# Kernel tuning notes

Hardware: AMD Instinct MI355X
Metric: run time of the kernel (lower is better)

Reference implementation:

```python
import jax, jax.numpy as jnp
import numpy as np

B, C, D_IN, T = 8, 4, 256, 1024
D_MODEL = 256


def setup_inputs() -> dict:
    key = jax.random.key(0)
    k_x, k_m, k_wq, k_bq, k_wo, k_bo = jax.random.split(key, 6)
    x = jax.random.normal(k_x, (B, C, D_IN, T), dtype=jnp.float32)
    mask = jax.random.randint(k_m, (B, C, T, T), 0, 2) == 1  # bool, True = masked
    s_in = 1.0 / np.sqrt(D_IN)
    s_md = 1.0 / np.sqrt(D_MODEL)
    w_qkv = jax.random.uniform(k_wq, (3 * D_MODEL, D_IN), jnp.float32, -s_in, s_in)
    b_qkv = jax.random.uniform(k_bq, (3 * D_MODEL,), jnp.float32, -s_in, s_in)
    w_out = jax.random.uniform(k_wo, (D_MODEL, D_MODEL), jnp.float32, -s_md, s_md)
    b_out = jax.random.uniform(k_bo, (D_MODEL,), jnp.float32, -s_md, s_md)
    return {"x": x, "mask": mask, "w_qkv": w_qkv, "b_qkv": b_qkv,
            "w_out": w_out, "b_out": b_out}


def reference(x, mask, w_qkv, b_qkv, w_out, b_out):
    # x: (B, C, d_in, t) -> (B, C, t, d_in)
    xt = jnp.swapaxes(x, -1, -2)
    qkv = jnp.einsum('bctd,ed->bcte', xt, w_qkv) + b_qkv  # (B,C,t,3*d_model)
    q, k, v = jnp.split(qkv, 3, axis=-1)
    scale = 1.0 / jnp.sqrt(jnp.asarray(q.shape[-1], dtype=q.dtype))
    scores = jnp.einsum('bcqd,bckd->bcqk', q, k) * scale  # (B,C,t,t)
    scores = jnp.where(mask, -jnp.inf, scores)
    attn = jax.nn.softmax(scores, axis=-1)
    out = jnp.einsum('bcqk,bckd->bcqd', attn, v)          # (B,C,t,d_model)
    return jnp.einsum('bcqd,ed->bcqe', out, w_out) + b_out
```

## Files before the change

### kernel.cpp

```cpp
#include <hip/hip_runtime.h>
#include <hip/hip_bf16.h>

#define TT 1024
#define DM 256
#define BCN 32

typedef __attribute__((ext_vector_type(8))) short short8;
typedef __attribute__((ext_vector_type(4))) short short4v;
typedef __attribute__((ext_vector_type(4))) float f32x4;

__device__ __forceinline__ void wg_barrier_lds() {
  asm volatile("s_waitcnt lgkmcnt(0)\n\ts_barrier" ::: "memory");
}

__device__ __forceinline__ short bf16b(float f) {
  __hip_bfloat16 h = __float2bfloat16(f);
  return *(short*)&h;
}

__device__ __forceinline__ void dma16(void* l, const void* g) {
  __builtin_amdgcn_global_load_lds(
      (const __attribute__((address_space(1))) void*)g,
      (__attribute__((address_space(3))) void*)l, 16, 0, 0);
}
__device__ __forceinline__ void dma4(void* l, const void* g) {
  __builtin_amdgcn_global_load_lds(
      (const __attribute__((address_space(1))) void*)g,
      (__attribute__((address_space(3))) void*)l, 4, 0, 0);
}

__global__ __launch_bounds__(256, 2) void qkv_kernel(
    const float* __restrict__ x, const float* __restrict__ w_qkv,
    const float* __restrict__ b_qkv, const int* __restrict__ mask,
    __hip_bfloat16* __restrict__ Qb, __hip_bfloat16* __restrict__ Kb,
    __hip_bfloat16* __restrict__ Vtb, unsigned* __restrict__ mbits)
{
  const int tid = threadIdx.x;

  if (blockIdx.x >= 512) {
    const int g = (blockIdx.x - 512) * 256 + tid;
#pragma unroll
    for (int k = 0; k < 8; ++k) {
      const int word = g + k * 131072;
      const int bc = word >> 15, j = (word >> 10) & 31, q = word & 1023;
      const int4* mp =
          (const int4*)(mask + ((size_t)(bc * 1024 + q) * 1024 + j * 32));
      unsigned w = 0;
#pragma unroll
      for (int i = 0; i < 8; ++i) {
        const int4 v = mp[i];
        w |= ((unsigned)(v.x != 0) << (4 * i)) |
             ((unsigned)(v.y != 0) << (4 * i + 1)) |
             ((unsigned)(v.z != 0) << (4 * i + 2)) |
             ((unsigned)(v.w != 0) << (4 * i + 3));
      }
      mbits[word] = w;
    }
    return;
  }

  const int tt = blockIdx.x & 15, bc = blockIdx.x >> 4;
  const int t0 = tt * 64;

  __shared__ __attribute__((aligned(16))) __hip_bfloat16 Xs[64][264];
  __shared__ __attribute__((aligned(16))) __hip_bfloat16 Ws[64][264];

  const int w = tid >> 6, l = tid & 63, quad = l >> 4, lm = l & 15;
  const float* xbc = x + (size_t)bc * DM * TT;

  {
    const int t4 = (tid & 15) * 4;
    for (int s = 0; s < 4; ++s) {
      const int d4 = (tid >> 4) * 4 + s * 64;
      f32x4 f[4];
#pragma unroll
      for (int r = 0; r < 4; ++r)
        f[r] = *(const f32x4*)(xbc + (size_t)(d4 + r) * TT + t0 + t4);
#pragma unroll
      for (int r = 0; r < 4; ++r) {
        short4v pk;
#pragma unroll
        for (int c = 0; c < 4; ++c) pk[c] = bf16b(f[c][r]);
        *(short4v*)&Xs[t4 + r][d4] = pk;
      }
    }
  }

  const float4* wv4 = (const float4*)w_qkv;

  for (int et = 0; et < 12; ++et) {
    const int e0 = et * 64;
    const bool vmode = (et >= 8);
    wg_barrier_lds();
#pragma unroll
    for (int i = 0; i < 16; ++i) {
      const int idx = tid + i * 256, row = idx >> 6, c4 = idx & 63;
      const float4 f = wv4[(size_t)et * 4096 + idx];
      short4v pk;
      pk[0] = bf16b(f.x); pk[1] = bf16b(f.y);
      pk[2] = bf16b(f.z); pk[3] = bf16b(f.w);
      *(short4v*)&Ws[row][c4 * 4] = pk;
    }
    wg_barrier_lds();

    f32x4 acc[4] = {};
#pragma unroll
    for (int ks = 0; ks < 8; ++ks) {
      const int k = ks * 32 + quad * 8;
      const short8 xa = *(const short8*)&Xs[w * 16 + lm][k];
#pragma unroll
      for (int nt = 0; nt < 4; ++nt) {
        const short8 wb = *(const short8*)&Ws[nt * 16 + lm][k];
        acc[nt] = vmode
            ? __builtin_amdgcn_mfma_f32_16x16x32_bf16(xa, wb, acc[nt], 0, 0, 0)
            : __builtin_amdgcn_mfma_f32_16x16x32_bf16(wb, xa, acc[nt], 0, 0, 0);
      }
    }

    if (et < 4) {
      const int t = t0 + w * 16 + lm;
#pragma unroll
      for (int nt = 0; nt < 4; ++nt) {
        const int ebase = e0 + nt * 16 + quad * 4;
        short4v pk;
#pragma unroll
        for (int r = 0; r < 4; ++r) pk[r] = bf16b(acc[nt][r] + b_qkv[ebase + r]);
        *(short4v*)&Qb[((size_t)bc * TT + t) * DM + ebase] = pk;
      }
    } else if (!vmode) {
      const int t = t0 + w * 16 + lm;
#pragma unroll
      for (int nt = 0; nt < 4; ++nt) {
        const int eg = e0 + nt * 16 + quad * 4;
        const int eK = eg - 256;
        short4v pk;
#pragma unroll
        for (int r = 0; r < 4; ++r) pk[r] = bf16b(acc[nt][r] + b_qkv[eg + r]);
        const int ch = eK >> 3;
        const int off = (((ch ^ (t & 7)) << 3) | (eK & 7));
        *(short4v*)&Kb[((size_t)bc * TT + t) * DM + off] = pk;
      }
    } else {
      const int tb = w * 16 + quad * 4;
      const int kb = tt * 2 + (tb >> 5), tloc = tb & 31;
#pragma unroll
      for (int nt = 0; nt < 4; ++nt) {
        const int e = (e0 - 512) + nt * 16 + lm;
        const float bq = b_qkv[512 + e];
        short4v pk;
#pragma unroll
        for (int r = 0; r < 4; ++r) pk[r] = bf16b(acc[nt][r] + bq);
        *(short4v*)&Vtb[(((size_t)bc * 32 + kb) * 256 + e) * 32 + tloc] = pk;
      }
    }
  }
}

__global__ __launch_bounds__(256, 2) void attn_kernel(
    const __hip_bfloat16* __restrict__ Qb, const __hip_bfloat16* __restrict__ Kb,
    const __hip_bfloat16* __restrict__ Vtb, const unsigned* __restrict__ Mbits,
    __hip_bfloat16* __restrict__ Ob)
{
  const int fid = blockIdx.x;
  const int xcd = fid & 7, slot = fid >> 3;
  const int bc = xcd * 4 + (slot >> 4);
  const int qt = slot & 15;
  const int q0 = qt * 64;

  __shared__ __attribute__((aligned(16))) __hip_bfloat16 Ks[2][32 * 256];
  __shared__ __attribute__((aligned(16))) __hip_bfloat16 Vs[2][256 * 32];
  __shared__ __attribute__((aligned(16))) __hip_bfloat16 Ps[64][40];
  __shared__ unsigned Msb[2][64];

  const int tid = threadIdx.x, w = tid >> 6, l = tid & 63;
  const int quad = l >> 4, lm = l & 15, lm7 = lm & 7;

  const __hip_bfloat16* Qg =
      Qb + ((size_t)bc * TT + q0 + w * 16 + lm) * DM + quad * 8;
  short8 qf[8];
#pragma unroll
  for (int ks = 0; ks < 8; ++ks) qf[ks] = *(const short8*)(Qg + ks * 32);

  const char* KgT = (const char*)(Kb + (size_t)bc * TT * DM);
  const char* VgT = (const char*)(Vtb + (size_t)bc * TT * DM);
  const unsigned* MgT = Mbits + ((size_t)bc * 32) * 1024 + q0;

  short8 ones;
#pragma unroll
  for (int i = 0; i < 8; ++i) ones[i] = (short)0x3F80;

  f32x4 Oa[16] = {};
  f32x4 Ol = {};

  auto issue = [&](int j, int buf) {
    const char* kg = KgT + (size_t)j * 16384 + w * 4096 + l * 16;
    const char* vg = VgT + (size_t)j * 16384 + w * 4096 + l * 16;
    char* kl = (char*)&Ks[buf][0] + w * 4096;
    char* vl = (char*)&Vs[buf][0] + w * 4096;
#pragma unroll
    for (int i = 0; i < 4; ++i) dma16(kl + i * 1024, kg + i * 1024);
#pragma unroll
    for (int i = 0; i < 4; ++i) dma16(vl + i * 1024, vg + i * 1024);
    dma4(&Msb[buf][0], MgT + (size_t)j * 1024 + l);
  };

  auto compute = [&](int buf) {
    const __hip_bfloat16* KT = &Ks[buf][0];
    const __hip_bfloat16* VT = &Vs[buf][0];
    f32x4 Sa0 = {}, Sa1 = {};
#pragma unroll
    for (int ks = 0; ks < 8; ++ks) {
      const int c = ((ks * 4 + quad) ^ lm7) << 3;
      const short8 a0 = *(const short8*)&KT[lm * 256 + c];
      const short8 a1 = *(const short8*)&KT[(lm + 16) * 256 + c];
      Sa0 = __builtin_amdgcn_mfma_f32_16x16x32_bf16(a0, qf[ks], Sa0, 0, 0, 0);
      Sa1 = __builtin_amdgcn_mfma_f32_16x16x32_bf16(a1, qf[ks], Sa1, 0, 0, 0);
    }
    const unsigned mw = Msb[buf][w * 16 + lm];
#pragma unroll
    for (int nt = 0; nt < 2; ++nt) {
      const f32x4 Sa = nt ? Sa1 : Sa0;
      short4v pk;
#pragma unroll
      for (int r = 0; r < 4; ++r) {
        const int jj = nt * 16 + quad * 4 + r;
        const float p = ((mw >> jj) & 1u)
                            ? 0.f
                            : __expf(fmaf(Sa[r], 0.0625f, -8.0f));
        pk[r] = bf16b(p);
      }
      *(short4v*)&Ps[w * 16 + lm][nt * 16 + quad * 4] = pk;
    }
    const short8 pf = *(const short8*)&Ps[w * 16 + lm][quad * 8];
#pragma unroll
    for (int ct = 0; ct < 16; ++ct) {
      const short8 a = *(const short8*)&VT[(ct * 16 + lm) * 32 + quad * 8];
      Oa[ct] = __builtin_amdgcn_mfma_f32_16x16x32_bf16(a, pf, Oa[ct], 0, 0, 0);
    }
    Ol = __builtin_amdgcn_mfma_f32_16x16x32_bf16(ones, pf, Ol, 0, 0, 0);
  };

  issue(0, 0);
  issue(1, 1);
#pragma unroll 1
  for (int j = 0; j < 32; ++j) {
    const int buf = j & 1;
    if (j < 31)
      asm volatile("s_waitcnt vmcnt(9)" ::: "memory");
    else
      asm volatile("s_waitcnt vmcnt(0)" ::: "memory");
    asm volatile("s_barrier" ::: "memory");
    compute(buf);
    wg_barrier_lds();
    if (j < 30) issue(j + 2, buf);
  }

  const float inv = 1.0f / Ol[0];
  __hip_bfloat16* Og = Ob + ((size_t)bc * TT + q0 + w * 16 + lm) * DM;
#pragma unroll
  for (int ct = 0; ct < 16; ++ct) {
    short4v pk;
#pragma unroll
    for (int r = 0; r < 4; ++r) pk[r] = bf16b(Oa[ct][r] * inv);
    *(short4v*)&Og[ct * 16 + quad * 4] = pk;
  }
}

__global__ __launch_bounds__(256, 2) void proj_kernel(
    const __hip_bfloat16* __restrict__ Ob, const float* __restrict__ w_out,
    const float* __restrict__ b_out, float* __restrict__ out)
{
  const int ft = blockIdx.x, tt = blockIdx.y, bc = blockIdx.z;
  const int f0 = ft * 64, t0 = tt * 64;

  __shared__ __attribute__((aligned(16))) __hip_bfloat16 As[64][264];
  __shared__ __attribute__((aligned(16))) __hip_bfloat16 Bs[64][264];

  const int tid = threadIdx.x;
  const uint4* Og4 = (const uint4*)(Ob + ((size_t)bc * TT + t0) * DM);
#pragma unroll
  for (int i = 0; i < 8; ++i) {
    const int chunk = tid + i * 256, row = chunk >> 5, c8 = chunk & 31;
    *(uint4*)&As[row][c8 * 8] = Og4[chunk];
  }
  {
    const float4* wv = (const float4*)(w_out + (size_t)f0 * DM);
#pragma unroll
    for (int i = 0; i < 16; ++i) {
      const int idx = tid + i * 256, row = idx >> 6, c4 = idx & 63;
      const float4 f = wv[idx];
      short4v pk;
      pk[0] = bf16b(f.x); pk[1] = bf16b(f.y);
      pk[2] = bf16b(f.z); pk[3] = bf16b(f.w);
      *(short4v*)&Bs[row][c4 * 4] = pk;
    }
  }
  __syncthreads();

  const int w = tid >> 6, l = tid & 63, quad = l >> 4, lm = l & 15;
  f32x4 acc[4] = {};
#pragma unroll
  for (int ks = 0; ks < 8; ++ks) {
    const int k = ks * 32 + quad * 8;
    const short8 ob = *(const short8*)&As[w * 16 + lm][k];
#pragma unroll
    for (int nt = 0; nt < 4; ++nt) {
      const short8 wa = *(const short8*)&Bs[nt * 16 + lm][k];
      acc[nt] = __builtin_amdgcn_mfma_f32_16x16x32_bf16(wa, ob, acc[nt], 0, 0, 0);
    }
  }
  const int t = t0 + w * 16 + lm;
#pragma unroll
  for (int nt = 0; nt < 4; ++nt) {
    const int fb = f0 + nt * 16 + quad * 4;
    float4 o;
    o.x = acc[nt][0] + b_out[fb + 0];
    o.y = acc[nt][1] + b_out[fb + 1];
    o.z = acc[nt][2] + b_out[fb + 2];
    o.w = acc[nt][3] + b_out[fb + 3];
    *(float4*)&out[((size_t)bc * TT + t) * DM + fb] = o;
  }
}

extern "C" void kernel_launch(void* const* d_in, const int* in_sizes, int n_in,
                              void* d_out, int out_size, void* d_ws, size_t ws_size,
                              hipStream_t stream) {
  const float* x = (const float*)d_in[0];
  const int* mask = (const int*)d_in[1];
  const float* w_qkv = (const float*)d_in[2];
  const float* b_qkv = (const float*)d_in[3];
  const float* w_out = (const float*)d_in[4];
  const float* b_out = (const float*)d_in[5];
  float* out = (float*)d_out;

  const size_t N = (size_t)BCN * TT * DM;
  __hip_bfloat16* Qb  = (__hip_bfloat16*)d_ws;
  __hip_bfloat16* Kb  = Qb + N;
  __hip_bfloat16* Vtb = Kb + N;
  unsigned* Mbits     = (unsigned*)(Vtb + N);

  qkv_kernel<<<dim3(1024), dim3(256), 0, stream>>>(x, w_qkv, b_qkv, mask,
                                                   Qb, Kb, Vtb, Mbits);
  attn_kernel<<<dim3(512), dim3(256), 0, stream>>>(Qb, Kb, Vtb, Mbits, Qb);
  proj_kernel<<<dim3(4, 16, BCN), dim3(256), 0, stream>>>(Qb, w_out, b_out, out);
}
```

Baseline: 361.5 us.

## Prepack weights to bf16, read weights from global directly, ballot-based mask packing

```diff
diff --git a/kernel.cpp b/kernel.cpp
--- a/kernel.cpp
+++ b/kernel.cpp
@@ -29,32 +29,53 @@
       (__attribute__((address_space(3))) void*)l, 4, 0, 0);
 }
 
-__global__ __launch_bounds__(256, 2) void qkv_kernel(
-    const float* __restrict__ x, const float* __restrict__ w_qkv,
-    const float* __restrict__ b_qkv, const int* __restrict__ mask,
-    __hip_bfloat16* __restrict__ Qb, __hip_bfloat16* __restrict__ Kb,
-    __hip_bfloat16* __restrict__ Vtb, unsigned* __restrict__ mbits)
+__global__ __launch_bounds__(256) void prepack_kernel(
+    const float* __restrict__ wq, const float* __restrict__ wo,
+    __hip_bfloat16* __restrict__ wqb, __hip_bfloat16* __restrict__ wob)
+{
+  const int t = blockIdx.x * 256 + threadIdx.x;
+#pragma unroll
+  for (int i = 0; i < 4; ++i) {
+    const int idx = t + i * 16384;
+    float4 f;
+    __hip_bfloat16* dst;
+    int di;
+    if (idx < 49152) { f = ((const float4*)wq)[idx]; dst = wqb; di = idx; }
+    else { f = ((const float4*)wo)[idx - 49152]; dst = wob; di = idx - 49152; }
+    short4v pk;
+    pk[0] = bf16b(f.x); pk[1] = bf16b(f.y);
+    pk[2] = bf16b(f.z); pk[3] = bf16b(f.w);
+    *(short4v*)&dst[di * 4] = pk;
+  }
+}
+
+__global__ __launch_bounds__(256) __attribute__((amdgpu_waves_per_eu(4, 4)))
+void qkv_kernel(const float* __restrict__ x,
+                const __hip_bfloat16* __restrict__ wqb,
+                const float* __restrict__ b_qkv, const int* __restrict__ mask,
+                __hip_bfloat16* __restrict__ Qb, __hip_bfloat16* __restrict__ Kb,
+                __hip_bfloat16* __restrict__ Vtb, unsigned* __restrict__ mbits)
 {
   const int tid = threadIdx.x;
+  const int w = tid >> 6, l = tid & 63, quad = l >> 4, lm = l & 15;
 
   if (blockIdx.x >= 512) {
-    const int g = (blockIdx.x - 512) * 256 + tid;
-#pragma unroll
-    for (int k = 0; k < 8; ++k) {
-      const int word = g + k * 131072;
-      const int bc = word >> 15, j = (word >> 10) & 31, q = word & 1023;
-      const int4* mp =
-          (const int4*)(mask + ((size_t)(bc * 1024 + q) * 1024 + j * 32));
-      unsigned w = 0;
-#pragma unroll
-      for (int i = 0; i < 8; ++i) {
-        const int4 v = mp[i];
-        w |= ((unsigned)(v.x != 0) << (4 * i)) |
-             ((unsigned)(v.y != 0) << (4 * i + 1)) |
-             ((unsigned)(v.z != 0) << (4 * i + 2)) |
-             ((unsigned)(v.w != 0) << (4 * i + 3));
-      }
-      mbits[word] = w;
+    const int b = blockIdx.x - 512;
+    const int bc = b >> 3;
+    const int q0 = (b & 7) * 128 + w * 32;
+    const int* base = mask + (size_t)bc * TT * TT;
+    for (int qi = 0; qi < 32; ++qi) {
+      const int q = q0 + qi;
+      const int* row = base + (size_t)q * TT + l;
+#pragma unroll
+      for (int j2 = 0; j2 < 16; ++j2) {
+        const int v = row[j2 * 64];
+        const unsigned long long bal = __ballot(v != 0);
+        if (l == 0)
+          mbits[((size_t)bc * 32 + j2 * 2) * 1024 + q] = (unsigned)bal;
+        if (l == 32)
+          mbits[((size_t)bc * 32 + j2 * 2 + 1) * 1024 + q] = (unsigned)(bal >> 32);
+      }
     }
     return;
   }
@@ -63,9 +84,6 @@
   const int t0 = tt * 64;
 
   __shared__ __attribute__((aligned(16))) __hip_bfloat16 Xs[64][264];
-  __shared__ __attribute__((aligned(16))) __hip_bfloat16 Ws[64][264];
-
-  const int w = tid >> 6, l = tid & 63, quad = l >> 4, lm = l & 15;
   const float* xbc = x + (size_t)bc * DM * TT;
 
   {
@@ -85,35 +103,27 @@
       }
     }
   }
-
-  const float4* wv4 = (const float4*)w_qkv;
-
+  __syncthreads();
+
+  short8 xf[8];
+#pragma unroll
+  for (int ks = 0; ks < 8; ++ks)
+    xf[ks] = *(const short8*)&Xs[w * 16 + lm][ks * 32 + quad * 8];
+
+#pragma unroll 1
   for (int et = 0; et < 12; ++et) {
     const int e0 = et * 64;
     const bool vmode = (et >= 8);
-    wg_barrier_lds();
-#pragma unroll
-    for (int i = 0; i < 16; ++i) {
-      const int idx = tid + i * 256, row = idx >> 6, c4 = idx & 63;
-      const float4 f = wv4[(size_t)et * 4096 + idx];
-      short4v pk;
-      pk[0] = bf16b(f.x); pk[1] = bf16b(f.y);
-      pk[2] = bf16b(f.z); pk[3] = bf16b(f.w);
-      *(short4v*)&Ws[row][c4 * 4] = pk;
-    }
-    wg_barrier_lds();
-
     f32x4 acc[4] = {};
 #pragma unroll
     for (int ks = 0; ks < 8; ++ks) {
-      const int k = ks * 32 + quad * 8;
-      const short8 xa = *(const short8*)&Xs[w * 16 + lm][k];
-#pragma unroll
-      for (int nt = 0; nt < 4; ++nt) {
-        const short8 wb = *(const short8*)&Ws[nt * 16 + lm][k];
+#pragma unroll
+      for (int nt = 0; nt < 4; ++nt) {
+        const short8 wb = *(const short8*)(wqb +
+            (size_t)(e0 + nt * 16 + lm) * DM + ks * 32 + quad * 8);
         acc[nt] = vmode
-            ? __builtin_amdgcn_mfma_f32_16x16x32_bf16(xa, wb, acc[nt], 0, 0, 0)
-            : __builtin_amdgcn_mfma_f32_16x16x32_bf16(wb, xa, acc[nt], 0, 0, 0);
+            ? __builtin_amdgcn_mfma_f32_16x16x32_bf16(xf[ks], wb, acc[nt], 0, 0, 0)
+            : __builtin_amdgcn_mfma_f32_16x16x32_bf16(wb, xf[ks], acc[nt], 0, 0, 0);
       }
     }
 
@@ -266,59 +276,56 @@
   }
 }
 
-__global__ __launch_bounds__(256, 2) void proj_kernel(
-    const __hip_bfloat16* __restrict__ Ob, const float* __restrict__ w_out,
-    const float* __restrict__ b_out, float* __restrict__ out)
+__global__ __launch_bounds__(256) __attribute__((amdgpu_waves_per_eu(4, 4)))
+void proj_kernel(const __hip_bfloat16* __restrict__ Ob,
+                 const __hip_bfloat16* __restrict__ wob,
+                 const float* __restrict__ b_out, float* __restrict__ out)
 {
-  const int ft = blockIdx.x, tt = blockIdx.y, bc = blockIdx.z;
-  const int f0 = ft * 64, t0 = tt * 64;
+  const int tt = blockIdx.x & 15, bc = blockIdx.x >> 4;
+  const int t0 = tt * 64;
 
   __shared__ __attribute__((aligned(16))) __hip_bfloat16 As[64][264];
-  __shared__ __attribute__((aligned(16))) __hip_bfloat16 Bs[64][264];
 
   const int tid = threadIdx.x;
+  const int w = tid >> 6, l = tid & 63, quad = l >> 4, lm = l & 15;
+
   const uint4* Og4 = (const uint4*)(Ob + ((size_t)bc * TT + t0) * DM);
 #pragma unroll
   for (int i = 0; i < 8; ++i) {
     const int chunk = tid + i * 256, row = chunk >> 5, c8 = chunk & 31;
     *(uint4*)&As[row][c8 * 8] = Og4[chunk];
   }
-  {
-    const float4* wv = (const float4*)(w_out + (size_t)f0 * DM);
-#pragma unroll
-    for (int i = 0; i < 16; ++i) {
-      const int idx = tid + i * 256, row = idx >> 6, c4 = idx & 63;
-      const float4 f = wv[idx];
-      short4v pk;
-      pk[0] = bf16b(f.x); pk[1] = bf16b(f.y);
-      pk[2] = bf16b(f.z); pk[3] = bf16b(f.w);
-      *(short4v*)&Bs[row][c4 * 4] = pk;
-    }
-  }
   __syncthreads();
 
-  const int w = tid >> 6, l = tid & 63, quad = l >> 4, lm = l & 15;
-  f32x4 acc[4] = {};
-#pragma unroll
-  for (int ks = 0; ks < 8; ++ks) {
-    const int k = ks * 32 + quad * 8;
-    const short8 ob = *(const short8*)&As[w * 16 + lm][k];
+  short8 of[8];
+#pragma unroll
+  for (int ks = 0; ks < 8; ++ks)
+    of[ks] = *(const short8*)&As[w * 16 + lm][ks * 32 + quad * 8];
+
+#pragma unroll 1
+  for (int ft = 0; ft < 4; ++ft) {
+    const int f0 = ft * 64;
+    f32x4 acc[4] = {};
+#pragma unroll
+    for (int ks = 0; ks < 8; ++ks) {
+#pragma unroll
+      for (int nt = 0; nt < 4; ++nt) {
+        const short8 wa = *(const short8*)(wob +
+            (size_t)(f0 + nt * 16 + lm) * DM + ks * 32 + quad * 8);
+        acc[nt] = __builtin_amdgcn_mfma_f32_16x16x32_bf16(wa, of[ks], acc[nt], 0, 0, 0);
+      }
+    }
+    const int t = t0 + w * 16 + lm;
 #pragma unroll
     for (int nt = 0; nt < 4; ++nt) {
-      const short8 wa = *(const short8*)&Bs[nt * 16 + lm][k];
-      acc[nt] = __builtin_amdgcn_mfma_f32_16x16x32_bf16(wa, ob, acc[nt], 0, 0, 0);
-    }
-  }
-  const int t = t0 + w * 16 + lm;
-#pragma unroll
-  for (int nt = 0; nt < 4; ++nt) {
-    const int fb = f0 + nt * 16 + quad * 4;
-    float4 o;
-    o.x = acc[nt][0] + b_out[fb + 0];
-    o.y = acc[nt][1] + b_out[fb + 1];
-    o.z = acc[nt][2] + b_out[fb + 2];
-    o.w = acc[nt][3] + b_out[fb + 3];
-    *(float4*)&out[((size_t)bc * TT + t) * DM + fb] = o;
+      const int fb = f0 + nt * 16 + quad * 4;
+      float4 o;
+      o.x = acc[nt][0] + b_out[fb + 0];
+      o.y = acc[nt][1] + b_out[fb + 1];
+      o.z = acc[nt][2] + b_out[fb + 2];
+      o.w = acc[nt][3] + b_out[fb + 3];
+      *(float4*)&out[((size_t)bc * TT + t) * DM + fb] = o;
+    }
   }
 }
 
@@ -338,9 +345,12 @@
   __hip_bfloat16* Kb  = Qb + N;
   __hip_bfloat16* Vtb = Kb + N;
   unsigned* Mbits     = (unsigned*)(Vtb + N);
-
-  qkv_kernel<<<dim3(1024), dim3(256), 0, stream>>>(x, w_qkv, b_qkv, mask,
-                                                   Qb, Kb, Vtb, Mbits);
+  __hip_bfloat16* wqb = (__hip_bfloat16*)(Mbits + (1u << 20));
+  __hip_bfloat16* wob = wqb + 768 * 256;
+
+  prepack_kernel<<<dim3(64), dim3(256), 0, stream>>>(w_qkv, w_out, wqb, wob);
+  qkv_kernel<<<dim3(768), dim3(256), 0, stream>>>(x, wqb, b_qkv, mask,
+                                                  Qb, Kb, Vtb, Mbits);
   attn_kernel<<<dim3(512), dim3(256), 0, stream>>>(Qb, Kb, Vtb, Mbits, Qb);
-  proj_kernel<<<dim3(4, 16, BCN), dim3(256), 0, stream>>>(Qb, w_out, b_out, out);
-}
+  proj_kernel<<<dim3(512), dim3(256), 0, stream>>>(Qb, wob, b_out, out);
+}
```

Result: slower. 548.0 us (+51.6%).
